# Performance work log

Hardware: AMD Instinct MI355X
Metric: run time of the kernel (lower is better)

The kernel has to match this reference:

```python
import jax, jax.numpy as jnp
import numpy as np

EPS = 1e-8

def _address(h, w_prev, mem, Wk, bk, Wb, bb, Wg, bg, Ws, bs, Wgam, bgam):
    # h: [B,H], w_prev: [B,N], mem: [B,N,M]
    k = jnp.tanh(h @ Wk + bk)                                 # key        [B,M]
    beta = jax.nn.softplus(h @ Wb + bb)[:, None]              # strength   [B,1]
    g = jax.nn.sigmoid(h @ Wg + bg)[:, None]                  # gate       [B,1]
    s = jax.nn.softmax(h @ Ws + bs, axis=-1)                  # shift      [B,3]
    gamma = 1.0 + jax.nn.softplus(h @ Wgam + bgam)[:, None]   # sharpen    [B,1]
    # content addressing: cosine similarity
    dot = jnp.einsum('bm,bnm->bn', k, mem)                    # [B,N]
    sim = dot / (jnp.linalg.norm(k, axis=-1, keepdims=True) * jnp.linalg.norm(mem, axis=-1) + EPS)
    wc = jax.nn.softmax(beta * sim, axis=-1)
    # gated interpolation with previous weights
    wg_ = g * wc + (1.0 - g) * w_prev
    # circular convolution with 3-tap shift kernel (-1, 0, +1)
    shifted = (s[:, 0:1] * jnp.roll(wg_, 1, axis=-1)
               + s[:, 1:2] * wg_
               + s[:, 2:3] * jnp.roll(wg_, -1, axis=-1))
    # sharpening
    wp = shifted ** gamma
    return wp / (jnp.sum(wp, axis=-1, keepdims=True) + EPS)


def reference(x, mem0, wr0, ww0, h0, Wx, Wrd, bh, Wk, bk, Wb, bb, Wg, bg, Ws, bs, Wgam, bgam, We, be, Wa, ba):
    B = x.shape[0]
    mem_init = jnp.broadcast_to(mem0, (B,) + mem0.shape)  # [B,N,M]

    def step(carry, x_t):
        mem, wr, ww, h = carry
        # write to memory using previous hidden state and previous write weights
        erase = jax.nn.sigmoid(h @ We + be)               # [B,M]
        add = jnp.tanh(h @ Wa + ba)                       # [B,M]
        mem = mem * (1.0 - ww[:, :, None] * erase[:, None, :]) + ww[:, :, None] * add[:, None, :]
        # read from updated memory with previous read weights
        r = jnp.einsum('bn,bnm->bm', wr, mem)             # [B,M]
        # controller step
        h = jnp.tanh(x_t @ Wx + r @ Wrd + bh)             # [B,H]
        # update addressing weights (head 0 = read, head 1 = write)
        wr_n = _address(h, wr, mem, Wk[0], bk[0], Wb[0], bb[0], Wg[0], bg[0], Ws[0], bs[0], Wgam[0], bgam[0])
        ww_n = _address(h, ww, mem, Wk[1], bk[1], Wb[1], bb[1], Ws is None, bg[1], Ws[1], bs[1], Wgam[1], bgam[1]) if False else _address(h, ww, mem, Wk[1], bk[1], Wb[1], bb[1], Wg[1], bg[1], Ws[1], bs[1], Wgam[1], bgam[1])
        return (mem, wr_n, ww_n, h), h

    _, hids = jax.lax.scan(step, (mem_init, wr0, ww0, h0), jnp.swapaxes(x, 0, 1))
    return jnp.swapaxes(hids, 0, 1)  # [B,T,H]


def setup_inputs() -> dict:
    key = jax.random.key(0)
    B, T, D, N, M, H = 128, 128, 128, 128, 128, 256
    ks = jax.random.split(key, 16)
    sc = 0.1
    wr0 = jnp.zeros((B, N), jnp.float32).at[:, 0].set(1.0)
    return {
        'x':    jax.random.normal(ks[0], (B, T, D), jnp.float32),
        'mem0': jax.random.uniform(ks[1], (N, M), jnp.float32) * 0.1,
        'wr0':  wr0,
        'ww0':  wr0,
        'h0':   jnp.zeros((B, H), jnp.float32),
        'Wx':   jax.random.normal(ks[2], (D, H), jnp.float32) * sc,
        'Wrd':  jax.random.normal(ks[3], (M, H), jnp.float32) * sc,
        'bh':   jnp.zeros((H,), jnp.float32),
        'Wk':   jax.random.normal(ks[4], (2, H, M), jnp.float32) * sc,
        'bk':   jnp.zeros((2, M), jnp.float32),
        'Wb':   jax.random.normal(ks[5], (2, H), jnp.float32) * sc,
        'bb':   jnp.zeros((2,), jnp.float32),
        'Wg':   jax.random.normal(ks[6], (2, H), jnp.float32) * sc,
        'bg':   jnp.zeros((2,), jnp.float32),
        'Ws':   jax.random.normal(ks[7], (2, H, 3), jnp.float32) * sc,
        'bs':   jnp.zeros((2, 3), jnp.float32),
        'Wgam': jax.random.normal(ks[8], (2, H), jnp.float32) * sc,
        'bgam': jnp.zeros((2,), jnp.float32),
        'We':   jax.random.normal(ks[9], (H, M), jnp.float32) * sc,
        'be':   jnp.zeros((M,), jnp.float32),
        'Wa':   jax.random.normal(ks[10], (H, M), jnp.float32) * sc,
        'ba':   jnp.zeros((M,), jnp.float32),
    }
```

## Files before the change

### kernel.cpp

```cpp
#include <hip/hip_runtime.h>
#include <math.h>

#define Tt 128
#define NT 512
#define EPSF 1e-8f

typedef _Float16 f16x2 __attribute__((ext_vector_type(2)));

__device__ __forceinline__ float fsigmoid(float v) { return 1.f / (1.f + expf(-v)); }
__device__ __forceinline__ float fsoftplus(float v) { return (v > 20.f) ? v : log1pf(expf(v)); }
__device__ __forceinline__ float ftanh(float v) { float e = expf(2.f * v); return 1.f - 2.f / (e + 1.f); }

__device__ __forceinline__ float dot2(f16x2 a, f16x2 b, float c) {
#if __has_builtin(__builtin_amdgcn_fdot2)
  return __builtin_amdgcn_fdot2(a, b, c, false);
#else
  return c + (float)a.x * (float)b.x + (float)a.y * (float)b.y;
#endif
}
__device__ __forceinline__ f16x2 pack2(float a, float b) {
  f16x2 p; p.x = (_Float16)a; p.y = (_Float16)b; return p;
}
__device__ __forceinline__ f16x2 bc16(unsigned int v) { return __builtin_bit_cast(f16x2, v); }

template <int C> __device__ __forceinline__ float dppadd(float v) {
  int s = __builtin_amdgcn_update_dpp(0, __builtin_bit_cast(int, v), C, 0xf, 0xf, true);
  return v + __builtin_bit_cast(float, s);
}
template <int C> __device__ __forceinline__ float dppmax(float v) {
  int iv = __builtin_bit_cast(int, v);
  int s = __builtin_amdgcn_update_dpp(iv, iv, C, 0xf, 0xf, false);
  return fmaxf(v, __builtin_bit_cast(float, s));
}
__device__ __forceinline__ float qsum16(float v) {
  v = dppadd<0x111>(v); v = dppadd<0x112>(v); v = dppadd<0x114>(v); v = dppadd<0x118>(v);
  return v;
}
__device__ __forceinline__ float halfsum(float v) {
  v = qsum16(v); v = dppadd<0x142>(v);
  return v;
}
__device__ __forceinline__ float allsum(float v) {
  v = halfsum(v); v = dppadd<0x143>(v);
  return __builtin_bit_cast(float, __builtin_amdgcn_readlane(__builtin_bit_cast(int, v), 63));
}
__device__ __forceinline__ float allmax(float v) {
  v = dppmax<0x111>(v); v = dppmax<0x112>(v); v = dppmax<0x114>(v);
  v = dppmax<0x118>(v); v = dppmax<0x142>(v); v = dppmax<0x143>(v);
  return __builtin_bit_cast(float, __builtin_amdgcn_readlane(__builtin_bit_cast(int, v), 63));
}

__global__ __launch_bounds__(512, 1) void ntm_prep(
    const float* __restrict__ We, const float* __restrict__ Wa,
    const float* __restrict__ Wk, unsigned int* __restrict__ wsb)
{
  const int i = blockIdx.x * 512 + threadIdx.x;
  const int e = i & 3;
  const int col = (i >> 2) & 511;
  const int q = i >> 11;
  const int k0 = 8 * q + 2 * e;
  const int mat = col >> 7;
  const int mcol = col & 127;
  const float* base = (mat == 0) ? We : (mat == 1) ? Wa : (mat == 2) ? Wk : (Wk + 256 * 128);
  wsb[i] = __builtin_bit_cast(unsigned int,
             pack2(base[k0 * 128 + mcol], base[(k0 + 1) * 128 + mcol]));
}

__global__ __launch_bounds__(NT, 1) void ntm_kernel(
    const float* __restrict__ x, const float* __restrict__ mem0,
    const float* __restrict__ wr0, const float* __restrict__ ww0,
    const float* __restrict__ h0, const float* __restrict__ Wx,
    const float* __restrict__ Wrd, const float* __restrict__ bh,
    const float* __restrict__ bk,
    const float* __restrict__ Wb, const float* __restrict__ bb,
    const float* __restrict__ Wg, const float* __restrict__ bg,
    const float* __restrict__ Ws, const float* __restrict__ bs,
    const float* __restrict__ Wgam, const float* __restrict__ bgam,
    const float* __restrict__ be, const float* __restrict__ ba,
    const uint4* __restrict__ wsb4,
    float* __restrict__ out)
{
  const int b = blockIdx.x;
  const int t = threadIdx.x;
  const int lane = t & 63;
  const int wave = t >> 6;
  const int cg = t & 63;
  const int js = t >> 6;
  const int c4 = t & 31;
  const int rs = t >> 5;

  __shared__ __align__(16) float mem[128 * 128];
  __shared__ __align__(16) uint4 lbigq[3584];
  __shared__ __align__(16) float part[2048];
  __shared__ __align__(16) float h_l[256];
  __shared__ __align__(16) unsigned int h16[128];
  __shared__ __align__(16) float xf[128];
  __shared__ __align__(16) float rf[128];
  __shared__ __align__(16) float er[128];
  __shared__ __align__(16) float ad[128];
  __shared__ __align__(16) float kbuf[256];
  __shared__ float wsm_l[3072];
  __shared__ float wr_s[128], ww_s[128];
  __shared__ float normsq[128];
  __shared__ float dotv[256];
  __shared__ float scal[12];
  __shared__ float red2[4];
  __shared__ float bias_big[512];
  __shared__ float bh_l[256];
  __shared__ float bias_sm[12];

  f16x2 wcreg[64];
  {
    const float* basep = (js < 4) ? (Wx + (js * 32) * 256) : (Wrd + ((js - 4) * 32) * 256);
    #pragma unroll
    for (int c = 0; c < 4; ++c) {
      const float* bp = basep + c * 64 + cg;
      #pragma unroll
      for (int jj = 0; jj < 16; ++jj) {
        wcreg[c * 16 + jj] = pack2(bp[(2 * jj) * 256], bp[(2 * jj + 1) * 256]);
      }
    }
  }

  for (int i = t; i < 128 * 128; i += NT) mem[i] = mem0[i];
  for (int i = t; i < 3584; i += NT) lbigq[i] = wsb4[12800 + i];
  if (t < 128) { wr_s[t] = wr0[b * 128 + t]; ww_s[t] = ww0[b * 128 + t]; }
  if (t < 256) {
    float v = h0[b * 256 + t];
    h_l[t] = v; bh_l[t] = bh[t];
    const float vo = __shfl_xor(v, 1);
    if (!(t & 1)) h16[t >> 1] = __builtin_bit_cast(unsigned int, pack2(v, vo));
  }
  bias_big[t] = (t < 128) ? be[t] : (t < 256) ? ba[t - 128] : bk[t - 256];
  for (int i = t; i < 3072; i += NT) {
    const int d = i >> 8, j = i & 255;
    const int head = d / 6, kind = d % 6;
    float v;
    if (kind == 0)      v = Wb[head * 256 + j];
    else if (kind == 1) v = Wg[head * 256 + j];
    else if (kind == 2) v = Wgam[head * 256 + j];
    else                v = Ws[head * 768 + j * 3 + (kind - 3)];
    wsm_l[i] = v;
  }
  if (t < 12) {
    const int head = t / 6, kind = t % 6;
    bias_sm[t] = (kind == 0) ? bb[head] : (kind == 1) ? bg[head]
               : (kind == 2) ? bgam[head] : bs[head * 3 + (kind - 3)];
  }
  __syncthreads();

  const uint4* h16_4 = reinterpret_cast<const uint4*>(h16);

  uint4 pf[4];
  auto issue_pf = [&]() {
    #pragma unroll
    for (int q = 0; q < 4; ++q) pf[q] = wsb4[q * 512 + t];
  };

  auto phase_big4 = [&]() {
    float a0 = 0.f, a1 = 0.f, a2 = 0.f, a3 = 0.f;
    #pragma unroll
    for (int q = 0; q < 32; ++q) {
      uint4 w;
      if (q < 4)        w = pf[q];
      else if (q >= 25) w = lbigq[(q - 25) * 512 + t];
      else              w = wsb4[q * 512 + t];
      const uint4 hq = h16_4[q];
      a0 = dot2(bc16(hq.x), bc16(w.x), a0);
      a1 = dot2(bc16(hq.y), bc16(w.y), a1);
      a2 = dot2(bc16(hq.z), bc16(w.z), a2);
      a3 = dot2(bc16(hq.w), bc16(w.w), a3);
    }
    const float acc = (a0 + a1) + (a2 + a3) + bias_big[t];
    if (t < 128)      er[t] = fsigmoid(acc);
    else if (t < 256) ad[t - 128] = ftanh(acc);
    else {
      const float kv = ftanh(acc);
      kbuf[t - 256] = kv;
      float ks = kv * kv;
      ks = halfsum(ks); ks = dppadd<0x143>(ks);
      if (lane == 63) red2[wave - 4] = ks;
    }
    if (t < 384) {
      const int d = t >> 5, l5 = t & 31;
      float s = 0.f;
      #pragma unroll
      for (int q = 0; q < 8; ++q) s += h_l[l5 + 32 * q] * wsm_l[d * 256 + l5 + 32 * q];
      s = halfsum(s);
      if ((lane & 31) == 31) scal[d] = s + bias_sm[d];
    }
  };

  issue_pf();
  phase_big4();
  __syncthreads();

  for (int step = 0; step < Tt; ++step) {
    issue_pf();

    if (t < 128) xf[t] = x[((size_t)b * Tt + step) * 128 + t];
    {
      const float4 e4 = *reinterpret_cast<const float4*>(&er[c4 * 4]);
      const float4 a4 = *reinterpret_cast<const float4*>(&ad[c4 * 4]);
      float rx = 0.f, ry = 0.f, rz = 0.f, rw = 0.f;
      #pragma unroll
      for (int k = 0; k < 8; ++k) {
        const int n = rs + 16 * k;
        const float wwn = ww_s[n], wrn = wr_s[n];
        float4 v = *reinterpret_cast<const float4*>(&mem[n * 128 + c4 * 4]);
        v.x = v.x * (1.f - wwn * e4.x) + wwn * a4.x;
        v.y = v.y * (1.f - wwn * e4.y) + wwn * a4.y;
        v.z = v.z * (1.f - wwn * e4.z) + wwn * a4.z;
        v.w = v.w * (1.f - wwn * e4.w) + wwn * a4.w;
        *reinterpret_cast<float4*>(&mem[n * 128 + c4 * 4]) = v;
        rx += wrn * v.x; ry += wrn * v.y; rz += wrn * v.z; rw += wrn * v.w;
      }
      *reinterpret_cast<float4*>(&part[rs * 128 + c4 * 4]) = make_float4(rx, ry, rz, rw);
    }
    __syncthreads();

    if (t < 128) {
      float r = 0.f;
      #pragma unroll
      for (int s = 0; s < 16; ++s) r += part[s * 128 + t];
      rf[t] = r;
    }
    __syncthreads();

    {
      const float* src = (js < 4) ? (xf + js * 32) : (rf + (js - 4) * 32);
      float acc[4];
      #pragma unroll
      for (int c = 0; c < 4; ++c) acc[c] = 0.f;
      #pragma unroll
      for (int jj = 0; jj < 16; ++jj) {
        const float2 s2 = *reinterpret_cast<const float2*>(&src[2 * jj]);
        const f16x2 xx = pack2(s2.x, s2.y);
        #pragma unroll
        for (int c = 0; c < 4; ++c) acc[c] = dot2(xx, wcreg[c * 16 + jj], acc[c]);
      }
      #pragma unroll
      for (int c = 0; c < 4; ++c) part[js * 256 + c * 64 + cg] = acc[c];
    }
    __syncthreads();

    if (t < 256) {
      float v = bh_l[t];
      #pragma unroll
      for (int s = 0; s < 8; ++s) v += part[s * 256 + t];
      v = ftanh(v);
      h_l[t] = v;
      out[((size_t)b * Tt + step) * 256 + t] = v;
      const float vo = __shfl_xor(v, 1);
      if (!(t & 1)) h16[t >> 1] = __builtin_bit_cast(unsigned int, pack2(v, vo));
    }
    __syncthreads();

    phase_big4();
    __syncthreads();

    {
      const int head = t >> 8;
      const int u = t & 255;
      const int cc = u & 31, ns = u >> 5;
      const float4 k4 = *reinterpret_cast<const float4*>(&kbuf[head * 128 + cc * 4]);
      #pragma unroll
      for (int ch = 0; ch < 2; ++ch) {
        float dsum[8], qsum[8];
        #pragma unroll
        for (int ii = 0; ii < 8; ++ii) {
          const int n = ns * 16 + ch * 8 + ii;
          const float4 m4 = *reinterpret_cast<const float4*>(&mem[n * 128 + cc * 4]);
          dsum[ii] = k4.x * m4.x + k4.y * m4.y + k4.z * m4.z + k4.w * m4.w;
          qsum[ii] = m4.x * m4.x + m4.y * m4.y + m4.z * m4.z + m4.w * m4.w;
        }
        #pragma unroll
        for (int ii = 0; ii < 8; ++ii) dsum[ii] = halfsum(dsum[ii]);
        if (head == 0) {
          #pragma unroll
          for (int ii = 0; ii < 8; ++ii) qsum[ii] = halfsum(qsum[ii]);
        }
        if ((lane & 31) == 31) {
          #pragma unroll
          for (int ii = 0; ii < 8; ++ii) dotv[head * 128 + ns * 16 + ch * 8 + ii] = dsum[ii];
          if (head == 0) {
            #pragma unroll
            for (int ii = 0; ii < 8; ++ii) normsq[ns * 16 + ch * 8 + ii] = qsum[ii];
          }
        }
      }
    }
    __syncthreads();

    if (wave < 2) {
      const int head = wave;
      const int h6 = head * 6;
      const float beta  = fsoftplus(scal[h6]);
      const float g     = fsigmoid(scal[h6 + 1]);
      const float gamma = 1.f + fsoftplus(scal[h6 + 2]);
      float e0 = scal[h6 + 3], e1 = scal[h6 + 4], e2 = scal[h6 + 5];
      const float mx3 = fmaxf(e0, fmaxf(e1, e2));
      float x0 = expf(e0 - mx3), x1 = expf(e1 - mx3), x2 = expf(e2 - mx3);
      const float si = 1.f / (x0 + x1 + x2);
      const float s0 = x0 * si, s1 = x1 * si, s2 = x2 * si;
      const float knorm = sqrtf(red2[2 * head] + red2[2 * head + 1]);
      float* wprev = head ? ww_s : wr_s;
      const int n0 = 2 * lane, n1 = 2 * lane + 1;
      float l0 = beta * dotv[head * 128 + n0] / (knorm * sqrtf(normsq[n0]) + EPSF);
      float l1 = beta * dotv[head * 128 + n1] / (knorm * sqrtf(normsq[n1]) + EPSF);
      const float mx = allmax(fmaxf(l0, l1));
      float q0 = expf(l0 - mx), q1 = expf(l1 - mx);
      const float inv = 1.f / allsum(q0 + q1);
      const float wg0 = g * q0 * inv + (1.f - g) * wprev[n0];
      const float wg1 = g * q1 * inv + (1.f - g) * wprev[n1];
      const float wgl = __shfl(wg1, (lane + 63) & 63);
      const float wgr = __shfl(wg0, (lane + 1) & 63);
      const float sh0 = s0 * wgl + s1 * wg0 + s2 * wg1;
      const float sh1 = s0 * wg0 + s1 * wg1 + s2 * wgr;
      const float wp0 = exp2f(gamma * log2f(sh0));
      const float wp1 = exp2f(gamma * log2f(sh1));
      const float itot = 1.f / (allsum(wp0 + wp1) + EPSF);
      wprev[n0] = wp0 * itot;
      wprev[n1] = wp1 * itot;
    }
    __syncthreads();
  }
}

extern "C" void kernel_launch(void* const* d_in, const int* in_sizes, int n_in,
                              void* d_out, int out_size, void* d_ws, size_t ws_size,
                              hipStream_t stream) {
  const float* x    = (const float*)d_in[0];
  const float* mem0 = (const float*)d_in[1];
  const float* wr0  = (const float*)d_in[2];
  const float* ww0  = (const float*)d_in[3];
  const float* h0   = (const float*)d_in[4];
  const float* Wx   = (const float*)d_in[5];
  const float* Wrd  = (const float*)d_in[6];
  const float* bh   = (const float*)d_in[7];
  const float* Wk   = (const float*)d_in[8];
  const float* bk   = (const float*)d_in[9];
  const float* Wb   = (const float*)d_in[10];
  const float* bb   = (const float*)d_in[11];
  const float* Wg   = (const float*)d_in[12];
  const float* bg   = (const float*)d_in[13];
  const float* Ws   = (const float*)d_in[14];
  const float* bs   = (const float*)d_in[15];
  const float* Wgam = (const float*)d_in[16];
  const float* bgam = (const float*)d_in[17];
  const float* We   = (const float*)d_in[18];
  const float* be   = (const float*)d_in[19];
  const float* Wa   = (const float*)d_in[20];
  const float* ba   = (const float*)d_in[21];
  float* out = (float*)d_out;
  unsigned int* wsb = (unsigned int*)d_ws;

  hipLaunchKernelGGL(ntm_prep, dim3(128), dim3(512), 0, stream, We, Wa, Wk, wsb);
  hipLaunchKernelGGL(ntm_kernel, dim3(128), dim3(NT), 0, stream,
                     x, mem0, wr0, ww0, h0, Wx, Wrd, bh, bk, Wb, bb,
                     Wg, bg, Ws, bs, Wgam, bgam, be, ba,
                     (const uint4*)wsb, out);
}
```

Measured before the change: 801.4 us.

## Pad memory rows, reduce read vector via DPP, pack x/r to fp16 once

Pads the per-block memory matrix in LDS to a row stride of 132 floats. The write/read phase is remapped so each 16-lane group covers one column quad across memory rows, which lets the read vector be reduced with DPP inside the wave. That removes the partial-sum buffer, one reduction pass and one __syncthreads per step. The x and r vectors are stored directly as packed fp16 pairs for the controller matvec, and the weight prefetch depth grows from 4 to 6 uint4 loads, raising register use and LDS footprint.

```diff
diff --git a/kernel.cpp b/kernel.cpp
--- a/kernel.cpp
+++ b/kernel.cpp
@@ -4,6 +4,7 @@
 #define Tt 128
 #define NT 512
 #define EPSF 1e-8f
+#define MSTR 132
 
 typedef _Float16 f16x2 __attribute__((ext_vector_type(2)));
 
@@ -22,6 +23,9 @@
   f16x2 p; p.x = (_Float16)a; p.y = (_Float16)b; return p;
 }
 __device__ __forceinline__ f16x2 bc16(unsigned int v) { return __builtin_bit_cast(f16x2, v); }
+__device__ __forceinline__ unsigned int pk2u(float a, float b) {
+  return __builtin_bit_cast(unsigned int, pack2(a, b));
+}
 
 template <int C> __device__ __forceinline__ float dppadd(float v) {
   int s = __builtin_amdgcn_update_dpp(0, __builtin_bit_cast(int, v), C, 0xf, 0xf, true);
@@ -62,8 +66,7 @@
   const int mat = col >> 7;
   const int mcol = col & 127;
   const float* base = (mat == 0) ? We : (mat == 1) ? Wa : (mat == 2) ? Wk : (Wk + 256 * 128);
-  wsb[i] = __builtin_bit_cast(unsigned int,
-             pack2(base[k0 * 128 + mcol], base[(k0 + 1) * 128 + mcol]));
+  wsb[i] = pk2u(base[k0 * 128 + mcol], base[(k0 + 1) * 128 + mcol]);
 }
 
 __global__ __launch_bounds__(NT, 1) void ntm_kernel(
@@ -86,16 +89,15 @@
   const int wave = t >> 6;
   const int cg = t & 63;
   const int js = t >> 6;
-  const int c4 = t & 31;
-  const int rs = t >> 5;
-
-  __shared__ __align__(16) float mem[128 * 128];
+  const int c4q = wave * 4 + (lane >> 4);
+  const int slice = lane & 15;
+
+  __shared__ __align__(16) float mem[128 * MSTR];
   __shared__ __align__(16) uint4 lbigq[3584];
   __shared__ __align__(16) float part[2048];
   __shared__ __align__(16) float h_l[256];
   __shared__ __align__(16) unsigned int h16[128];
-  __shared__ __align__(16) float xf[128];
-  __shared__ __align__(16) float rf[128];
+  __shared__ __align__(16) unsigned int xr16[128];
   __shared__ __align__(16) float er[128];
   __shared__ __align__(16) float ad[128];
   __shared__ __align__(16) float kbuf[256];
@@ -122,14 +124,14 @@
     }
   }
 
-  for (int i = t; i < 128 * 128; i += NT) mem[i] = mem0[i];
+  for (int i = t; i < 16384; i += NT) mem[(i >> 7) * MSTR + (i & 127)] = mem0[i];
   for (int i = t; i < 3584; i += NT) lbigq[i] = wsb4[12800 + i];
   if (t < 128) { wr_s[t] = wr0[b * 128 + t]; ww_s[t] = ww0[b * 128 + t]; }
   if (t < 256) {
     float v = h0[b * 256 + t];
     h_l[t] = v; bh_l[t] = bh[t];
     const float vo = __shfl_xor(v, 1);
-    if (!(t & 1)) h16[t >> 1] = __builtin_bit_cast(unsigned int, pack2(v, vo));
+    if (!(t & 1)) h16[t >> 1] = pk2u(v, vo);
   }
   bias_big[t] = (t < 128) ? be[t] : (t < 256) ? ba[t - 128] : bk[t - 256];
   for (int i = t; i < 3072; i += NT) {
@@ -151,10 +153,10 @@
 
   const uint4* h16_4 = reinterpret_cast<const uint4*>(h16);
 
-  uint4 pf[4];
+  uint4 pf[6];
   auto issue_pf = [&]() {
     #pragma unroll
-    for (int q = 0; q < 4; ++q) pf[q] = wsb4[q * 512 + t];
+    for (int q = 0; q < 6; ++q) pf[q] = wsb4[q * 512 + t];
   };
 
   auto phase_big4 = [&]() {
@@ -162,7 +164,7 @@
     #pragma unroll
     for (int q = 0; q < 32; ++q) {
       uint4 w;
-      if (q < 4)        w = pf[q];
+      if (q < 6)        w = pf[q];
       else if (q >= 25) w = lbigq[(q - 25) * 512 + t];
       else              w = wsb4[q * 512 + t];
       const uint4 hq = h16_4[q];
@@ -198,44 +200,42 @@
   for (int step = 0; step < Tt; ++step) {
     issue_pf();
 
-    if (t < 128) xf[t] = x[((size_t)b * Tt + step) * 128 + t];
+    if (t < 64) {
+      const float2 xv = reinterpret_cast<const float2*>(x + ((size_t)b * Tt + step) * 128)[t];
+      xr16[t] = pk2u(xv.x, xv.y);
+    }
     {
-      const float4 e4 = *reinterpret_cast<const float4*>(&er[c4 * 4]);
-      const float4 a4 = *reinterpret_cast<const float4*>(&ad[c4 * 4]);
+      const float4 e4 = *reinterpret_cast<const float4*>(&er[c4q * 4]);
+      const float4 a4 = *reinterpret_cast<const float4*>(&ad[c4q * 4]);
       float rx = 0.f, ry = 0.f, rz = 0.f, rw = 0.f;
       #pragma unroll
       for (int k = 0; k < 8; ++k) {
-        const int n = rs + 16 * k;
+        const int n = slice + 16 * k;
         const float wwn = ww_s[n], wrn = wr_s[n];
-        float4 v = *reinterpret_cast<const float4*>(&mem[n * 128 + c4 * 4]);
+        float4 v = *reinterpret_cast<const float4*>(&mem[n * MSTR + c4q * 4]);
         v.x = v.x * (1.f - wwn * e4.x) + wwn * a4.x;
         v.y = v.y * (1.f - wwn * e4.y) + wwn * a4.y;
         v.z = v.z * (1.f - wwn * e4.z) + wwn * a4.z;
         v.w = v.w * (1.f - wwn * e4.w) + wwn * a4.w;
-        *reinterpret_cast<float4*>(&mem[n * 128 + c4 * 4]) = v;
+        *reinterpret_cast<float4*>(&mem[n * MSTR + c4q * 4]) = v;
         rx += wrn * v.x; ry += wrn * v.y; rz += wrn * v.z; rw += wrn * v.w;
       }
-      *reinterpret_cast<float4*>(&part[rs * 128 + c4 * 4]) = make_float4(rx, ry, rz, rw);
-    }
-    __syncthreads();
-
-    if (t < 128) {
-      float r = 0.f;
-      #pragma unroll
-      for (int s = 0; s < 16; ++s) r += part[s * 128 + t];
-      rf[t] = r;
+      rx = qsum16(rx); ry = qsum16(ry); rz = qsum16(rz); rw = qsum16(rw);
+      if (slice == 15) {
+        xr16[64 + c4q * 2]     = pk2u(rx, ry);
+        xr16[64 + c4q * 2 + 1] = pk2u(rz, rw);
+      }
     }
     __syncthreads();
 
     {
-      const float* src = (js < 4) ? (xf + js * 32) : (rf + (js - 4) * 32);
+      const unsigned int* src16 = (js < 4) ? (xr16 + js * 16) : (xr16 + 64 + (js - 4) * 16);
       float acc[4];
       #pragma unroll
       for (int c = 0; c < 4; ++c) acc[c] = 0.f;
       #pragma unroll
       for (int jj = 0; jj < 16; ++jj) {
-        const float2 s2 = *reinterpret_cast<const float2*>(&src[2 * jj]);
-        const f16x2 xx = pack2(s2.x, s2.y);
+        const f16x2 xx = bc16(src16[jj]);
         #pragma unroll
         for (int c = 0; c < 4; ++c) acc[c] = dot2(xx, wcreg[c * 16 + jj], acc[c]);
       }
@@ -252,7 +252,7 @@
       h_l[t] = v;
       out[((size_t)b * Tt + step) * 256 + t] = v;
       const float vo = __shfl_xor(v, 1);
-      if (!(t & 1)) h16[t >> 1] = __builtin_bit_cast(unsigned int, pack2(v, vo));
+      if (!(t & 1)) h16[t >> 1] = pk2u(v, vo);
     }
     __syncthreads();
 
@@ -270,7 +270,7 @@
         #pragma unroll
         for (int ii = 0; ii < 8; ++ii) {
           const int n = ns * 16 + ch * 8 + ii;
-          const float4 m4 = *reinterpret_cast<const float4*>(&mem[n * 128 + cc * 4]);
+          const float4 m4 = *reinterpret_cast<const float4*>(&mem[n * MSTR + cc * 4]);
           dsum[ii] = k4.x * m4.x + k4.y * m4.y + k4.z * m4.z + k4.w * m4.w;
           qsum[ii] = m4.x * m4.x + m4.y * m4.y + m4.z * m4.z + m4.w * m4.w;
         }
```

Result: slower. 828.4 us (+3.4%).
